# Optimization experiments

Hardware: AMD Instinct MI355X
Metric: run time of the kernel (lower is better)

The kernel has to match this reference:

```python
import math
import jax, jax.numpy as jnp
import numpy as np

NUM_HEADS = 32
HIDDEN = 4096
HEAD_DIM = HIDDEN // NUM_HEADS  # 128
NEG_INF = -1e30


def _alibi_slopes(n: int) -> jnp.ndarray:
    cp2 = 2 ** math.floor(math.log2(n))
    base = 2.0 ** (-(2.0 ** (-(math.log2(cp2) - 3))))
    slopes = base ** np.arange(1, cp2 + 1, dtype=np.float64)
    if cp2 != n:
        extra_base = 2.0 ** (-(2.0 ** (-(math.log2(2 * cp2) - 3))))
        rem = min(cp2, n - cp2)
        extra = extra_base ** np.arange(1, 1 + 2 * rem, 2, dtype=np.float64)
        slopes = np.concatenate([slopes, extra])
    return jnp.asarray(slopes, dtype=jnp.float32)


def setup_inputs() -> dict:
    key = jax.random.key(0)
    k1, k2, k3 = jax.random.split(key, 3)
    B, S = 2, 2048
    hidden_states = jax.random.normal(k1, (B, S, HIDDEN), dtype=jnp.float32)
    Wqkv = jax.random.normal(k2, (HIDDEN, NUM_HEADS * HEAD_DIM + 2 * HEAD_DIM), dtype=jnp.float32) * 0.02
    Wo = jax.random.normal(k3, (HIDDEN, HIDDEN), dtype=jnp.float32) * 0.02
    return {"hidden_states": hidden_states, "Wqkv": Wqkv, "Wo": Wo}


def reference(hidden_states, Wqkv, Wo):
    B, S, H = hidden_states.shape
    nH, d = NUM_HEADS, HEAD_DIM
    scale = d ** -0.5

    qkv = hidden_states @ Wqkv                      # [B,S,nH*d + 2d]
    q = qkv[..., : nH * d].reshape(B, S, nH, d)     # [B,S,nH,d]
    k = qkv[..., nH * d: nH * d + d]                # [B,S,d] (single kv head, MQA)
    v = qkv[..., nH * d + d:]                       # [B,S,d]

    scores = jnp.einsum("bqhd,bkd->bhqk", q, k) * scale  # [B,nH,S,S]

    pos_q = jnp.arange(S)[:, None]
    pos_k = jnp.arange(S)[None, :]
    slopes = _alibi_slopes(nH)                       # [nH]
    alibi = slopes[:, None, None] * (pos_k - pos_q).astype(jnp.float32)  # [nH,S,S]
    causal = pos_k <= pos_q                          # [S,S]

    scores = jnp.where(causal[None, None], scores + alibi[None], NEG_INF)
    probs = jax.nn.softmax(scores, axis=-1)
    attn = jnp.einsum("bhqk,bkd->bqhd", probs, v).reshape(B, S, H)
    return attn @ Wo
```

## Files before the change

### kernel.cpp

```cpp
#include <hip/hip_runtime.h>
#include <hip/hip_bf16.h>

typedef __attribute__((ext_vector_type(8))) short bf16x8;
typedef __attribute__((ext_vector_type(4))) float f32x4;
typedef __attribute__((ext_vector_type(8))) unsigned short u16x8;

__device__ __forceinline__ unsigned short f2bf(float x) {
    union { float f; unsigned u; } v; v.f = x;
    unsigned r = v.u + 0x7fff + ((v.u >> 16) & 1);
    return (unsigned short)(r >> 16);
}

__device__ __forceinline__ void gload16(const void* g, void* l) {
    __builtin_amdgcn_global_load_lds(
        (const __attribute__((address_space(1))) void*)g,
        (__attribute__((address_space(3))) void*)l, 16, 0, 0);
}

__global__ __launch_bounds__(256) void cast_bf16_kernel(
    const float* __restrict__ src, unsigned short* __restrict__ dst, int n8) {
    int i = blockIdx.x * 256 + threadIdx.x;
    if (i >= n8) return;
    const float4* s = (const float4*)src + (size_t)i * 2;
    float4 a = s[0], b = s[1];
    u16x8 o;
    o[0] = f2bf(a.x); o[1] = f2bf(a.y); o[2] = f2bf(a.z); o[3] = f2bf(a.w);
    o[4] = f2bf(b.x); o[5] = f2bf(b.y); o[6] = f2bf(b.z); o[7] = f2bf(b.w);
    *(u16x8*)(dst + (size_t)i * 8) = o;
}

__global__ __launch_bounds__(256) void transpose_cast_kernel(
    const float* __restrict__ src, unsigned short* __restrict__ dst, int R, int C) {
    __shared__ float tile[32][33];
    const int bx = blockIdx.x * 32, by = blockIdx.y * 32;
    const int tx = threadIdx.x & 31, ty = threadIdx.x >> 5;
#pragma unroll
    for (int i = 0; i < 32; i += 8)
        tile[ty + i][tx] = src[(size_t)(by + ty + i) * C + (bx + tx)];
    __syncthreads();
#pragma unroll
    for (int i = 0; i < 32; i += 8)
        dst[(size_t)(bx + ty + i) * R + (by + tx)] = f2bf(tile[tx][ty + i]);
}

template <int OUTBF>
__global__ __launch_bounds__(256) void gemm_kernel(
    const unsigned short* __restrict__ A, const unsigned short* __restrict__ BT,
    void* __restrict__ Cp, int M, int N, int K) {
    __shared__ unsigned short Al[2][128 * 32];
    __shared__ unsigned short Bl[2][128 * 32];
    const int t = threadIdx.x;
    const int wid = t >> 6, lane = t & 63;
    const int l15 = lane & 15, lg = lane >> 4;
    const int bm = blockIdx.y * 128, bn = blockIdx.x * 128;
    const int wm = (wid >> 1) * 64, wn = (wid & 1) * 64;

    f32x4 acc[4][4];
#pragma unroll
    for (int i = 0; i < 4; ++i)
#pragma unroll
        for (int j = 0; j < 4; ++j) acc[i][j] = (f32x4)(0.f);

    const int nk = K >> 5;
    const int c0 = t, c1 = t + 256;

    auto stage = [&](int buf, int kt) {
        const unsigned short* Ab = A + (size_t)bm * K + kt * 32;
        const unsigned short* Bb = BT + (size_t)bn * K + kt * 32;
        gload16(Ab + (size_t)(c0 >> 2) * K + (c0 & 3) * 8, &Al[buf][wid * 64 * 8]);
        gload16(Ab + (size_t)(c1 >> 2) * K + (c1 & 3) * 8, &Al[buf][(256 + wid * 64) * 8]);
        gload16(Bb + (size_t)(c0 >> 2) * K + (c0 & 3) * 8, &Bl[buf][wid * 64 * 8]);
        gload16(Bb + (size_t)(c1 >> 2) * K + (c1 & 3) * 8, &Bl[buf][(256 + wid * 64) * 8]);
    };

    stage(0, 0);
    __syncthreads();
    for (int kt = 0; kt < nk; ++kt) {
        const int cur = kt & 1;
        if (kt + 1 < nk) stage(cur ^ 1, kt + 1);
        bf16x8 af[4], bfr[4];
#pragma unroll
        for (int i = 0; i < 4; ++i) {
            af[i]  = *(const bf16x8*)&Al[cur][(wm + i * 16 + l15) * 32 + lg * 8];
            bfr[i] = *(const bf16x8*)&Bl[cur][(wn + i * 16 + l15) * 32 + lg * 8];
        }
#pragma unroll
        for (int i = 0; i < 4; ++i)
#pragma unroll
            for (int j = 0; j < 4; ++j)
                acc[i][j] = __builtin_amdgcn_mfma_f32_16x16x32_bf16(af[i], bfr[j], acc[i][j], 0, 0, 0);
        __syncthreads();
    }

#pragma unroll
    for (int i = 0; i < 4; ++i)
#pragma unroll
        for (int j = 0; j < 4; ++j)
#pragma unroll
            for (int r = 0; r < 4; ++r) {
                const int row = bm + wm + i * 16 + lg * 4 + r;
                const int col = bn + wn + j * 16 + l15;
                if (OUTBF) ((unsigned short*)Cp)[(size_t)row * N + col] = f2bf(acc[i][j][r]);
                else       ((float*)Cp)[(size_t)row * N + col] = acc[i][j][r];
            }
}

__global__ __launch_bounds__(256, 4) void attn_kernel(
    const unsigned short* __restrict__ qkv, unsigned short* __restrict__ attn, int S) {
    constexpr int LD = 4352;
    __shared__ unsigned short Kl[64 * 128];
    __shared__ unsigned short Vt[128 * 64];
    __shared__ unsigned short Pl[4][16 * 64];
    const int t = threadIdx.x, wid = t >> 6;
    const int lane = t & 63, l15 = lane & 15, lg = lane >> 4;
    const int h = blockIdx.y, b = blockIdx.z;
    const size_t rb = (size_t)b * S;
    const int nQB = S >> 6;
    const float scale2 = 0.08838834764831845f * 1.4426950408889634f;
    const float slope2 = exp2f(-0.25f * (float)(h + 1)) * 1.4426950408889634f;

    for (int half = 0; half < 2; ++half) {
        const int qblk = half ? (nQB - 1 - (int)blockIdx.x) : (int)blockIdx.x;
        const int q0 = qblk * 64 + wid * 16;

        bf16x8 qf[4];
        {
            const unsigned short* qrow = qkv + (rb + q0 + l15) * LD + h * 128 + lg * 8;
#pragma unroll
            for (int j = 0; j < 4; ++j) qf[j] = *(const bf16x8*)(qrow + j * 32);
        }
        f32x4 o[8];
#pragma unroll
        for (int i = 0; i < 8; ++i) o[i] = (f32x4)(0.f);
        float m_[4], l_[4];
#pragma unroll
        for (int r = 0; r < 4; ++r) { m_[r] = -1e30f; l_[r] = 0.f; }

        const int ntile = qblk + 1;
        for (int tile = 0; tile < ntile; ++tile) {
            const int t0 = tile * 64;
            {
                const char* kbase = (const char*)(qkv + (rb + t0) * LD + 4096);
#pragma unroll
                for (int i = 0; i < 4; ++i) {
                    const int c = i * 256 + t;
                    const int krow = c >> 4;
                    gload16(kbase + (size_t)krow * (LD * 2) + (((c & 15) * 16) ^ ((krow & 7) << 4)),
                            (char*)Kl + (i * 256 + wid * 64) * 16);
                }
            }
            {
                const unsigned short* vs = qkv + (rb + t0 + lane) * LD + 4224 + wid * 32;
                u16x8 v0 = *(const u16x8*)vs;
                u16x8 v1 = *(const u16x8*)(vs + 8);
                u16x8 v2 = *(const u16x8*)(vs + 16);
                u16x8 v3 = *(const u16x8*)(vs + 24);
                const int kb = 2 * lane;
#pragma unroll
                for (int e = 0; e < 8; ++e) {
                    int dd = wid * 32 + e;
                    *(unsigned short*)((char*)Vt + dd * 128 + (kb ^ ((dd & 7) << 4))) = v0[e];
                    dd += 8;
                    *(unsigned short*)((char*)Vt + dd * 128 + (kb ^ ((dd & 7) << 4))) = v1[e];
                    dd += 8;
                    *(unsigned short*)((char*)Vt + dd * 128 + (kb ^ ((dd & 7) << 4))) = v2[e];
                    dd += 8;
                    *(unsigned short*)((char*)Vt + dd * 128 + (kb ^ ((dd & 7) << 4))) = v3[e];
                }
            }
            __syncthreads();

            f32x4 s4[4];
#pragma unroll
            for (int ct = 0; ct < 4; ++ct) {
                s4[ct] = (f32x4)(0.f);
                const int row = ct * 16 + l15;
                const int swz = (row & 7) << 4;
#pragma unroll
                for (int j = 0; j < 4; ++j) {
                    bf16x8 kf = *(const bf16x8*)((const char*)Kl + row * 256 +
                                                 ((j * 64 + lg * 16) ^ swz));
                    s4[ct] = __builtin_amdgcn_mfma_f32_16x16x32_bf16(qf[j], kf, s4[ct], 0, 0, 0);
                }
            }

            float corr[4];
#pragma unroll
            for (int r = 0; r < 4; ++r) {
                const int q = q0 + lg * 4 + r;
                float sc[4];
#pragma unroll
                for (int ct = 0; ct < 4; ++ct) {
                    const int kv = t0 + ct * 16 + l15;
                    sc[ct] = (kv <= q) ? s4[ct][r] * scale2 + slope2 * (float)(kv - q) : -1e30f;
                }
                float mx = fmaxf(fmaxf(sc[0], sc[1]), fmaxf(sc[2], sc[3]));
                mx = fmaxf(mx, __shfl_xor(mx, 1, 16));
                mx = fmaxf(mx, __shfl_xor(mx, 2, 16));
                mx = fmaxf(mx, __shfl_xor(mx, 4, 16));
                mx = fmaxf(mx, __shfl_xor(mx, 8, 16));
                const float mnew = fmaxf(m_[r], mx);
                corr[r] = exp2f(m_[r] - mnew);
                m_[r] = mnew;
                float p0 = exp2f(sc[0] - mnew), p1 = exp2f(sc[1] - mnew);
                float p2 = exp2f(sc[2] - mnew), p3 = exp2f(sc[3] - mnew);
                float rs = (p0 + p1) + (p2 + p3);
                rs += __shfl_xor(rs, 1, 16);
                rs += __shfl_xor(rs, 2, 16);
                rs += __shfl_xor(rs, 4, 16);
                rs += __shfl_xor(rs, 8, 16);
                l_[r] = l_[r] * corr[r] + rs;
                const int prow = lg * 4 + r;
                char* pb = (char*)&Pl[wid][0] + prow * 128;
                const int swz = (prow & 7) << 4;
                *(unsigned short*)(pb + ((2 * l15) ^ swz))      = f2bf(p0);
                *(unsigned short*)(pb + ((32 + 2 * l15) ^ swz)) = f2bf(p1);
                *(unsigned short*)(pb + ((64 + 2 * l15) ^ swz)) = f2bf(p2);
                *(unsigned short*)(pb + ((96 + 2 * l15) ^ swz)) = f2bf(p3);
            }

            const char* pb = (const char*)&Pl[wid][0] + l15 * 128;
            const int pswz = (l15 & 7) << 4;
            bf16x8 pa0 = *(const bf16x8*)(pb + ((lg * 16) ^ pswz));
            bf16x8 pa1 = *(const bf16x8*)(pb + ((64 + lg * 16) ^ pswz));
#pragma unroll
            for (int n = 0; n < 8; ++n) {
                const int dd = n * 16 + l15;
                const int vswz = (dd & 7) << 4;
                bf16x8 vf0 = *(const bf16x8*)((const char*)Vt + dd * 128 + ((lg * 16) ^ vswz));
                bf16x8 vf1 = *(const bf16x8*)((const char*)Vt + dd * 128 + ((64 + lg * 16) ^ vswz));
                f32x4 a4 = o[n];
                a4[0] *= corr[0]; a4[1] *= corr[1]; a4[2] *= corr[2]; a4[3] *= corr[3];
                a4 = __builtin_amdgcn_mfma_f32_16x16x32_bf16(pa0, vf0, a4, 0, 0, 0);
                a4 = __builtin_amdgcn_mfma_f32_16x16x32_bf16(pa1, vf1, a4, 0, 0, 0);
                o[n] = a4;
            }
            __syncthreads();
        }

        float rinv[4];
#pragma unroll
        for (int r = 0; r < 4; ++r) rinv[r] = 1.f / l_[r];
#pragma unroll
        for (int n = 0; n < 8; ++n)
#pragma unroll
            for (int r = 0; r < 4; ++r) {
                const int q = q0 + lg * 4 + r;
                attn[(rb + q) * 4096 + h * 128 + n * 16 + l15] = f2bf(o[n][r] * rinv[r]);
            }
    }
}

extern "C" void kernel_launch(void* const* d_in, const int* in_sizes, int n_in,
                              void* d_out, int out_size, void* d_ws, size_t ws_size,
                              hipStream_t stream) {
    const float* hidden = (const float*)d_in[0];
    const float* Wqkv   = (const float*)d_in[1];
    const float* Wo     = (const float*)d_in[2];
    float* out = (float*)d_out;
    char* ws = (char*)d_ws;

    const int B = 2, S = 2048, H = 4096, NQ = 4352;
    const int M = B * S;

    unsigned short* hb  = (unsigned short*)(ws);
    unsigned short* wT  = (unsigned short*)(ws + 33554432);
    unsigned short* qkv = (unsigned short*)(ws + 33554432 + 35651584);

    cast_bf16_kernel<<<(M * H / 8) / 256, 256, 0, stream>>>(hidden, hb, M * H / 8);
    transpose_cast_kernel<<<dim3(NQ / 32, H / 32), 256, 0, stream>>>(Wqkv, wT, H, NQ);
    gemm_kernel<1><<<dim3(NQ / 128, M / 128), 256, 0, stream>>>(hb, wT, qkv, M, NQ, H);
    transpose_cast_kernel<<<dim3(H / 32, H / 32), 256, 0, stream>>>(Wo, wT, H, H);
    attn_kernel<<<dim3(16, 32, 2), 256, 0, stream>>>(qkv, hb, S);
    gemm_kernel<0><<<dim3(H / 128, M / 128), 256, 0, stream>>>(hb, wT, out, M, H, H);
}
```

Before: 618.0 us.

## Transpose QK MFMA so each lane owns a query row; lazy softmax rescale

Swaps the MFMA operand order so S^T is computed and each lane holds one query row's scores. Row max and row sum then need only two cross-lane shuffles instead of four per row. Adds a lazy rescaling rule that skips the running-max update and output correction unless the new max exceeds the old by more than 8 (log2 units). It also applies the causal mask only on the diagonal tile, folds the ALiBi bias into precomputed per-lane offsets, and writes P with packed 4-element stores using the hardware bf16 conversion.

```diff
diff --git a/kernel.cpp b/kernel.cpp
--- a/kernel.cpp
+++ b/kernel.cpp
@@ -4,11 +4,17 @@
 typedef __attribute__((ext_vector_type(8))) short bf16x8;
 typedef __attribute__((ext_vector_type(4))) float f32x4;
 typedef __attribute__((ext_vector_type(8))) unsigned short u16x8;
+typedef __attribute__((ext_vector_type(4))) unsigned short u16x4;
 
 __device__ __forceinline__ unsigned short f2bf(float x) {
     union { float f; unsigned u; } v; v.f = x;
     unsigned r = v.u + 0x7fff + ((v.u >> 16) & 1);
     return (unsigned short)(r >> 16);
+}
+
+__device__ __forceinline__ unsigned short f2bf_hw(float x) {
+    __hip_bfloat16 h = __float2bfloat16(x);
+    return *reinterpret_cast<unsigned short*>(&h);
 }
 
 __device__ __forceinline__ void gload16(const void* g, void* l) {
@@ -118,23 +124,24 @@
     const int nQB = S >> 6;
     const float scale2 = 0.08838834764831845f * 1.4426950408889634f;
     const float slope2 = exp2f(-0.25f * (float)(h + 1)) * 1.4426950408889634f;
+    const float sr1 = slope2, sr2 = slope2 * 2.f, sr3 = slope2 * 3.f;
 
     for (int half = 0; half < 2; ++half) {
         const int qblk = half ? (nQB - 1 - (int)blockIdx.x) : (int)blockIdx.x;
-        const int q0 = qblk * 64 + wid * 16;
+        const int q0w = qblk * 64 + wid * 16;
+        const int qlane = q0w + l15;
+        const float aq = slope2 * (float)qlane;
 
         bf16x8 qf[4];
         {
-            const unsigned short* qrow = qkv + (rb + q0 + l15) * LD + h * 128 + lg * 8;
+            const unsigned short* qrow = qkv + (rb + qlane) * LD + h * 128 + lg * 8;
 #pragma unroll
             for (int j = 0; j < 4; ++j) qf[j] = *(const bf16x8*)(qrow + j * 32);
         }
         f32x4 o[8];
 #pragma unroll
         for (int i = 0; i < 8; ++i) o[i] = (f32x4)(0.f);
-        float m_[4], l_[4];
-#pragma unroll
-        for (int r = 0; r < 4; ++r) { m_[r] = -1e30f; l_[r] = 0.f; }
+        float m_ = -1e30f, l_ = 0.f;
 
         const int ntile = qblk + 1;
         for (int tile = 0; tile < ntile; ++tile) {
@@ -180,43 +187,68 @@
                 for (int j = 0; j < 4; ++j) {
                     bf16x8 kf = *(const bf16x8*)((const char*)Kl + row * 256 +
                                                  ((j * 64 + lg * 16) ^ swz));
-                    s4[ct] = __builtin_amdgcn_mfma_f32_16x16x32_bf16(qf[j], kf, s4[ct], 0, 0, 0);
-                }
-            }
-
-            float corr[4];
-#pragma unroll
-            for (int r = 0; r < 4; ++r) {
-                const int q = q0 + lg * 4 + r;
-                float sc[4];
+                    s4[ct] = __builtin_amdgcn_mfma_f32_16x16x32_bf16(kf, qf[j], s4[ct], 0, 0, 0);
+                }
+            }
+
+            const float base = slope2 * (float)(t0 + lg * 4) - aq;
+            float p4[4][4];
+            float mx = -1e30f;
+            const bool lastt = (tile == ntile - 1);
+            const int dbase = t0 + lg * 4 - qlane;
+#pragma unroll
+            for (int ct = 0; ct < 4; ++ct) {
+                const float bbc = base + slope2 * 16.f * (float)ct;
+#pragma unroll
+                for (int r = 0; r < 4; ++r) {
+                    float sc = fmaf(s4[ct][r], scale2,
+                                    bbc + (r == 0 ? 0.f : (r == 1 ? sr1 : (r == 2 ? sr2 : sr3))));
+                    if (lastt && (dbase + ct * 16 + r > 0)) sc = -1e30f;
+                    p4[ct][r] = sc;
+                    mx = fmaxf(mx, sc);
+                }
+            }
+            mx = fmaxf(mx, __shfl_xor(mx, 16));
+            mx = fmaxf(mx, __shfl_xor(mx, 32));
+
+            if (!__all(mx <= m_ + 8.0f)) {
+                const float mnew = fmaxf(m_, mx);
+                const float corr = exp2f(m_ - mnew);
+                m_ = mnew;
+                l_ *= corr;
+                float cr[4];
+#pragma unroll
+                for (int r = 0; r < 4; ++r) cr[r] = __shfl(corr, lg * 4 + r);
+#pragma unroll
+                for (int n = 0; n < 8; ++n) {
+                    o[n][0] *= cr[0]; o[n][1] *= cr[1];
+                    o[n][2] *= cr[2]; o[n][3] *= cr[3];
+                }
+            }
+
+            float rs = 0.f;
+#pragma unroll
+            for (int ct = 0; ct < 4; ++ct)
+#pragma unroll
+                for (int r = 0; r < 4; ++r) {
+                    const float pv = exp2f(p4[ct][r] - m_);
+                    p4[ct][r] = pv;
+                    rs += pv;
+                }
+            rs += __shfl_xor(rs, 16);
+            rs += __shfl_xor(rs, 32);
+            l_ += rs;
+
+            {
+                char* pb = (char*)&Pl[wid][0] + l15 * 128;
+                const int swz = (l15 & 7) << 4;
 #pragma unroll
                 for (int ct = 0; ct < 4; ++ct) {
-                    const int kv = t0 + ct * 16 + l15;
-                    sc[ct] = (kv <= q) ? s4[ct][r] * scale2 + slope2 * (float)(kv - q) : -1e30f;
-                }
-                float mx = fmaxf(fmaxf(sc[0], sc[1]), fmaxf(sc[2], sc[3]));
-                mx = fmaxf(mx, __shfl_xor(mx, 1, 16));
-                mx = fmaxf(mx, __shfl_xor(mx, 2, 16));
-                mx = fmaxf(mx, __shfl_xor(mx, 4, 16));
-                mx = fmaxf(mx, __shfl_xor(mx, 8, 16));
-                const float mnew = fmaxf(m_[r], mx);
-                corr[r] = exp2f(m_[r] - mnew);
-                m_[r] = mnew;
-                float p0 = exp2f(sc[0] - mnew), p1 = exp2f(sc[1] - mnew);
-                float p2 = exp2f(sc[2] - mnew), p3 = exp2f(sc[3] - mnew);
-                float rs = (p0 + p1) + (p2 + p3);
-                rs += __shfl_xor(rs, 1, 16);
-                rs += __shfl_xor(rs, 2, 16);
-                rs += __shfl_xor(rs, 4, 16);
-                rs += __shfl_xor(rs, 8, 16);
-                l_[r] = l_[r] * corr[r] + rs;
-                const int prow = lg * 4 + r;
-                char* pb = (char*)&Pl[wid][0] + prow * 128;
-                const int swz = (prow & 7) << 4;
-                *(unsigned short*)(pb + ((2 * l15) ^ swz))      = f2bf(p0);
-                *(unsigned short*)(pb + ((32 + 2 * l15) ^ swz)) = f2bf(p1);
-                *(unsigned short*)(pb + ((64 + 2 * l15) ^ swz)) = f2bf(p2);
-                *(unsigned short*)(pb + ((96 + 2 * l15) ^ swz)) = f2bf(p3);
+                    u16x4 w;
+                    w[0] = f2bf_hw(p4[ct][0]); w[1] = f2bf_hw(p4[ct][1]);
+                    w[2] = f2bf_hw(p4[ct][2]); w[3] = f2bf_hw(p4[ct][3]);
+                    *(u16x4*)(pb + ((ct * 32 + lg * 8) ^ swz)) = w;
+                }
             }
 
             const char* pb = (const char*)&Pl[wid][0] + l15 * 128;
@@ -229,24 +261,22 @@
                 const int vswz = (dd & 7) << 4;
                 bf16x8 vf0 = *(const bf16x8*)((const char*)Vt + dd * 128 + ((lg * 16) ^ vswz));
                 bf16x8 vf1 = *(const bf16x8*)((const char*)Vt + dd * 128 + ((64 + lg * 16) ^ vswz));
-                f32x4 a4 = o[n];
-                a4[0] *= corr[0]; a4[1] *= corr[1]; a4[2] *= corr[2]; a4[3] *= corr[3];
-                a4 = __builtin_amdgcn_mfma_f32_16x16x32_bf16(pa0, vf0, a4, 0, 0, 0);
-                a4 = __builtin_amdgcn_mfma_f32_16x16x32_bf16(pa1, vf1, a4, 0, 0, 0);
-                o[n] = a4;
+                f32x4 a4 = __builtin_amdgcn_mfma_f32_16x16x32_bf16(pa0, vf0, o[n], 0, 0, 0);
+                o[n] = __builtin_amdgcn_mfma_f32_16x16x32_bf16(pa1, vf1, a4, 0, 0, 0);
             }
             __syncthreads();
         }
 
-        float rinv[4];
-#pragma unroll
-        for (int r = 0; r < 4; ++r) rinv[r] = 1.f / l_[r];
+        const float rl = 1.f / l_;
+        float rv[4];
+#pragma unroll
+        for (int r = 0; r < 4; ++r) rv[r] = __shfl(rl, lg * 4 + r);
 #pragma unroll
         for (int n = 0; n < 8; ++n)
 #pragma unroll
             for (int r = 0; r < 4; ++r) {
-                const int q = q0 + lg * 4 + r;
-                attn[(rb + q) * 4096 + h * 128 + n * 16 + l15] = f2bf(o[n][r] * rinv[r]);
+                const int q = q0w + lg * 4 + r;
+                attn[(rb + q) * 4096 + h * 128 + n * 16 + l15] = f2bf(o[n][r] * rv[r]);
             }
     }
 }
```

Measured after the change: 555.4 us. -10.1%, faster.
